# Performance work log

Hardware: AMD Instinct MI355X
Metric: run time of the kernel (lower is better)

The kernel has to match this reference:

```python
import jax, jax.numpy as jnp
import numpy as np


def _conv_bn_relu(x, w, b, stride):
    # Conv2d(k=3, pad=1) with eval-mode BatchNorm folded into (w, b) at setup, then ReLU.
    y = jax.lax.conv_general_dilated(x, w, (stride, stride), ((1, 1), (1, 1)),
                                     dimension_numbers=('NCHW', 'OIHW', 'NCHW'))
    return jax.nn.relu(y + b[None, :, None, None])


def _affine_grid(theta, H, W):
    # torch.nn.functional.affine_grid, align_corners=False
    xs = (2.0 * jnp.arange(W, dtype=theta.dtype) + 1.0) / W - 1.0  # [W]
    ys = (2.0 * jnp.arange(H, dtype=theta.dtype) + 1.0) / H - 1.0  # [H]
    gx = theta[:, 0, 0, None, None] * xs[None, None, :] + theta[:, 0, 1, None, None] * ys[None, :, None] + theta[:, 0, 2, None, None]
    gy = theta[:, 1, 0, None, None] * xs[None, None, :] + theta[:, 1, 1, None, None] * ys[None, :, None] + theta[:, 1, 2, None, None]
    return jnp.stack([gx, gy], axis=-1)  # [B,H,W,2]


def _grid_sample_bilinear_zeros(im, grid):
    # torch.nn.functional.grid_sample, mode='bilinear', padding_mode='zeros', align_corners=False
    B, C, H, W = im.shape
    ix = ((grid[..., 0] + 1.0) * W - 1.0) * 0.5  # [B,H,W] pixel x coords
    iy = ((grid[..., 1] + 1.0) * H - 1.0) * 0.5
    x0 = jnp.floor(ix); y0 = jnp.floor(iy)
    x1 = x0 + 1.0;      y1 = y0 + 1.0
    wx1 = ix - x0; wx0 = 1.0 - wx1
    wy1 = iy - y0; wy0 = 1.0 - wy1
    imt = jnp.transpose(im, (0, 2, 3, 1))  # BHWC for channel-last gather
    bidx = jnp.arange(B)[:, None, None]

    def gather(xf, yf):
        valid = ((xf >= 0) & (xf <= W - 1) & (yf >= 0) & (yf <= H - 1)).astype(im.dtype)
        xi = jnp.clip(xf.astype(jnp.int32), 0, W - 1)
        yi = jnp.clip(yf.astype(jnp.int32), 0, H - 1)
        return imt[bidx, yi, xi] * valid[..., None]  # [B,H,W,C]

    out = (gather(x0, y0) * (wx0 * wy0)[..., None]
           + gather(x1, y0) * (wx1 * wy0)[..., None]
           + gather(x0, y1) * (wx0 * wy1)[..., None]
           + gather(x1, y1) * (wx1 * wy1)[..., None])
    return jnp.transpose(out, (0, 3, 1, 2))  # back to NCHW


def _forward(im_tensor, w1, b1, w2, b2, w3, b3, w4, b4, w5, b5, w6, b6,
             fw1, fb1, fw2, fb2, fw3, fb3):
    B, _, H, W = im_tensor.shape
    x1 = _conv_bn_relu(im_tensor, w1, b1, 1)
    x2 = _conv_bn_relu(jnp.concatenate([x1, im_tensor], 1), w2, b2, 2)
    x3 = _conv_bn_relu(x2, w3, b3, 1)
    x4 = _conv_bn_relu(jnp.concatenate([x3, x2], 1), w4, b4, 2)
    x5 = _conv_bn_relu(x4, w5, b5, 1)
    xs = _conv_bn_relu(jnp.concatenate([x5, x4], 1), w6, b6, 2)
    xs = xs.reshape(B, -1)  # [B, 24*(H/8)*(W/8)]
    h = jax.nn.relu(xs @ fw1.T + fb1)
    h = jax.nn.relu(h @ fw2.T + fb2)
    sz = h @ fw3.T + fb3  # [B, 4]
    # mode == 'normal': vectorized theta construction (original loops over batch)
    theta = jnp.zeros((B, 2, 3), dtype=im_tensor.dtype)
    theta = theta.at[:, 0, 0].set(jax.nn.sigmoid(sz[:, 0]))
    theta = theta.at[:, 0, 2].set(jnp.tanh(sz[:, 2]))
    theta = theta.at[:, 1, 1].set(jax.nn.sigmoid(sz[:, 1]))
    theta = theta.at[:, 1, 2].set(jnp.tanh(sz[:, 3]))
    grid = _affine_grid(theta, H, W)
    im_cropped = _grid_sample_bilinear_zeros(im_tensor, grid)
    return im_cropped, theta


def setup_inputs() -> dict:
    key = jax.random.key(0)
    B, H, W = 32, 256, 256
    keys = iter(jax.random.split(key, 64))
    nk = lambda: next(keys)
    im = jax.random.normal(nk(), (B, 1, H, W), jnp.float32)

    def conv_params(cin, cout):
        w = jax.random.normal(nk(), (cout, cin, 3, 3), jnp.float32) * (1.0 / np.sqrt(cin * 9))
        b = jax.random.normal(nk(), (cout,), jnp.float32) * 0.01
        # eval-mode BatchNorm params, folded into conv weight/bias (exact same math)
        gamma = 1.0 + 0.1 * jax.random.normal(nk(), (cout,), jnp.float32)
        beta = 0.1 * jax.random.normal(nk(), (cout,), jnp.float32)
        mean = 0.1 * jax.random.normal(nk(), (cout,), jnp.float32)
        var = jnp.abs(1.0 + 0.1 * jax.random.normal(nk(), (cout,), jnp.float32))
        scale = gamma / jnp.sqrt(var + 1e-5)
        return w * scale[:, None, None, None], b * scale + (beta - mean * scale)

    w1, b1 = conv_params(1, 8)
    w2, b2 = conv_params(9, 8)
    w3, b3 = conv_params(8, 16)
    w4, b4 = conv_params(24, 16)
    w5, b5 = conv_params(16, 24)
    w6, b6 = conv_params(40, 24)
    feat = 24 * (H // 8) * (W // 8)
    fw1 = jax.random.normal(nk(), (1024, feat), jnp.float32) * (1.0 / np.sqrt(feat))
    fb1 = jnp.zeros((1024,), jnp.float32)
    fw2 = jax.random.normal(nk(), (32, 1024), jnp.float32) * (1.0 / np.sqrt(1024))
    fb2 = jnp.zeros((32,), jnp.float32)
    fw3 = jax.random.normal(nk(), (4, 32), jnp.float32) * 0.01  # small perturbation of zero-init
    fb3 = jnp.array([1.0, 1.0, 0.0, 0.0], jnp.float32)
    return dict(im_tensor=im, w1=w1, b1=b1, w2=w2, b2=b2, w3=w3, b3=b3,
                w4=w4, b4=b4, w5=w5, b5=b5, w6=w6, b6=b6,
                fw1=fw1, fb1=fb1, fw2=fw2, fb2=fb2, fw3=fw3, fb3=fb3)


def reference(im_tensor, w1, b1, w2, b2, w3, b3, w4, b4, w5, b5, w6, b6,
              fw1, fb1, fw2, fb2, fw3, fb3):
    return _forward(im_tensor, w1, b1, w2, b2, w3, b3, w4, b4, w5, b5, w6, b6,
                    fw1, fb1, fw2, fb2, fw3, fb3)
```

## Files before the change

### kernel.cpp

```cpp
#include <hip/hip_runtime.h>
#include <hip/hip_bf16.h>

template <int CIN1, int CIN2, int COUT, int CG, int CCH, int MINW>
__global__ __launch_bounds__(256, MINW) void convq_k(
    const float* __restrict__ in1, const float* __restrict__ in2,
    const float* __restrict__ w,
    const float* __restrict__ bias,
    float* __restrict__ out,
    int Hin, int Win)
{
    constexpr int CIN = CIN1 + CIN2;
    constexpr int NG  = COUT / CG;
    constexpr int NCH = CIN / CCH;
    constexpr int P   = 34;
    constexpr int NF4 = 10;
    constexpr int WL  = NF4 * 4;
    constexpr int E4  = CCH * P * NF4;
    constexpr int NLD = (E4 + 255) / 256;
    __shared__ __align__(16) float Xs[2][CCH][P][WL];

    const int Ho = Hin, Wo = Win;
    const int tpr = Wo / 32, tpc = Ho / 32;
    int bid = blockIdx.x;
    const int tx = bid % tpr; bid /= tpr;
    const int ty = bid % tpc; bid /= tpc;
    const int g  = bid % NG;  bid /= NG;
    const int b  = bid;
    const int cbase = g * CG;

    const int tid = threadIdx.x;
    const int lx = tid & 15, ly = tid >> 4;

    const int y0 = ty * 32 - 1;
    const int xA = tx * 32 - 4;
    const int HW = Hin * Win;

    float acc[CG][4];
#pragma unroll
    for (int co = 0; co < CG; ++co) {
        float bv = bias[cbase + co];
#pragma unroll
        for (int p = 0; p < 4; ++p) acc[co][p] = bv;
    }

    int cA[NLD], lOff[NLD], em[NLD];
    bool eok[NLD], rowk[NLD], f4[NLD];
    const float* b1p[NLD];
    const float* b2p[NLD];
#pragma unroll
    for (int l = 0; l < NLD; ++l) {
        int e = tid + l * 256;
        eok[l] = (e < E4);
        int ee = eok[l] ? e : 0;
        int c  = ee / (P * NF4), r = ee % (P * NF4);
        int py = r / NF4,        jx = r % NF4;
        cA[l]   = c;
        lOff[l] = ee;
        int gy = y0 + py, c0 = xA + jx * 4;
        rowk[l] = eok[l] && ((unsigned)gy < (unsigned)Hin);
        f4[l]   = (c0 >= 0) && (c0 + 4 <= Win);
        em[l] = 0;
#pragma unroll
        for (int e2 = 0; e2 < 4; ++e2)
            if ((unsigned)(c0 + e2) < (unsigned)Win) em[l] |= 1 << e2;
        b1p[l] = (const float*)((const char*)in1 +
                 ((ptrdiff_t)(b * CIN1 + c) * HW + (ptrdiff_t)gy * Win + c0)
                 * (ptrdiff_t)sizeof(float));
        b2p[l] = (CIN2 > 0)
            ? (const float*)((const char*)in2 +
                 ((ptrdiff_t)(b * CIN2 + c - CIN1) * HW + (ptrdiff_t)gy * Win + c0)
                 * (ptrdiff_t)sizeof(float))
            : b1p[l];
    }

    float4 stg[NLD];

    auto issue = [&](int cc) {
        const size_t adv = (size_t)cc * HW;
#pragma unroll
        for (int l = 0; l < NLD; ++l) {
            float4 v = {0.0f, 0.0f, 0.0f, 0.0f};
            if (rowk[l]) {
                int ci = cc + cA[l];
                const float* p = (CIN2 == 0 || ci < CIN1) ? (b1p[l] + adv)
                                                          : (b2p[l] + adv);
                if (f4[l]) {
                    v = *(const float4*)p;
                } else {
                    float* vp = reinterpret_cast<float*>(&v);
#pragma unroll
                    for (int e2 = 0; e2 < 4; ++e2)
                        if (em[l] & (1 << e2)) vp[e2] = p[e2];
                }
            }
            stg[l] = v;
        }
    };
    auto commit = [&](int bf) {
        float4* dst = (float4*)&Xs[0][0][0][0] + (size_t)bf * (CCH * P * NF4);
#pragma unroll
        for (int l = 0; l < NLD; ++l)
            if (eok[l]) dst[lOff[l]] = stg[l];
    };

    issue(0);
    commit(0);
    __syncthreads();

    const int cb = 2 * lx + 3;

    int buf = 0;
    for (int ch = 0; ch < NCH; ++ch) {
        if (ch + 1 < NCH) issue((ch + 1) * CCH);
#pragma unroll
        for (int c = 0; c < CCH; ++c) {
#pragma unroll
            for (int ky = 0; ky < 3; ++ky) {
                const float* x0 = &Xs[buf][c][2 * ly + ky][cb];
                const float* x1 = &Xs[buf][c][2 * ly + ky + 1][cb];
                float a0 = x0[0], a1 = x0[1], a2 = x0[2], a3 = x0[3];
                float b0 = x1[0], b1v = x1[1], b2v = x1[2], b3 = x1[3];
#pragma unroll
                for (int co = 0; co < CG; ++co) {
                    const float* wp = w +
                        ((size_t)(cbase + co) * CIN + ch * CCH + c) * 9 + ky * 3;
                    float w0 = wp[0], w1 = wp[1], w2 = wp[2];
                    acc[co][0] = fmaf(a0, w0, acc[co][0]);
                    acc[co][0] = fmaf(a1, w1, acc[co][0]);
                    acc[co][0] = fmaf(a2, w2, acc[co][0]);
                    acc[co][1] = fmaf(a1, w0, acc[co][1]);
                    acc[co][1] = fmaf(a2, w1, acc[co][1]);
                    acc[co][1] = fmaf(a3, w2, acc[co][1]);
                    acc[co][2] = fmaf(b0, w0, acc[co][2]);
                    acc[co][2] = fmaf(b1v, w1, acc[co][2]);
                    acc[co][2] = fmaf(b2v, w2, acc[co][2]);
                    acc[co][3] = fmaf(b1v, w0, acc[co][3]);
                    acc[co][3] = fmaf(b2v, w1, acc[co][3]);
                    acc[co][3] = fmaf(b3, w2, acc[co][3]);
                }
            }
        }
        if (ch + 1 < NCH) {
            commit(buf ^ 1);
            __syncthreads();
            buf ^= 1;
        }
    }

    const int oy = ty * 32 + 2 * ly;
    const int ox = tx * 32 + 2 * lx;
#pragma unroll
    for (int co = 0; co < CG; ++co)
#pragma unroll
        for (int dy = 0; dy < 2; ++dy) {
            float2 v;
            v.x = fmaxf(acc[co][dy * 2 + 0], 0.0f);
            v.y = fmaxf(acc[co][dy * 2 + 1], 0.0f);
            *(float2*)&out[((size_t)(b * COUT + cbase + co) * Ho + oy + dy) * Wo + ox] = v;
        }
}

template <int CIN1, int CIN2, int COUT, int CG, int STRIDE, int CCH, int MINW>
__global__ __launch_bounds__(256, MINW) void conv2p_k(
    const float* __restrict__ in1, const float* __restrict__ in2,
    const float* __restrict__ w,
    const float* __restrict__ bias,
    float* __restrict__ out,
    int Hin, int Win)
{
    constexpr int CIN = CIN1 + CIN2;
    constexpr int NG  = COUT / CG;
    constexpr int NCH = CIN / CCH;
    constexpr int P   = 16 * STRIDE + 2;
    constexpr int NF4 = (STRIDE == 1) ? 10 : 17;
    constexpr int WL  = NF4 * 4;
    constexpr int E4  = CCH * P * NF4;
    constexpr int NLD = (E4 + 255) / 256;
    __shared__ __align__(16) float Xs[2][CCH][P][WL];

    const int Ho = Hin / STRIDE, Wo = Win / STRIDE;
    const int tpr = Wo / 32, tpc = Ho / 16;
    int bid = blockIdx.x;
    const int tx = bid % tpr; bid /= tpr;
    const int ty = bid % tpc; bid /= tpc;
    const int g  = bid % NG;  bid /= NG;
    const int b  = bid;
    const int cbase = g * CG;

    const int tid = threadIdx.x;
    const int lx = tid & 15, ly = tid >> 4;

    const int y0 = ty * 16 * STRIDE - 1;
    const int xA = tx * 32 * STRIDE - 4;
    const int HW = Hin * Win;

    float2 acc[CG];
#pragma unroll
    for (int co = 0; co < CG; ++co) {
        float bv = bias[cbase + co];
        acc[co].x = bv; acc[co].y = bv;
    }

    int cA[NLD], lOff[NLD], em[NLD];
    bool eok[NLD], rowk[NLD], f4[NLD];
    const float* b1p[NLD];
    const float* b2p[NLD];
#pragma unroll
    for (int l = 0; l < NLD; ++l) {
        int e = tid + l * 256;
        eok[l] = (e < E4);
        int ee = eok[l] ? e : 0;
        int c  = ee / (P * NF4), r = ee % (P * NF4);
        int py = r / NF4,        jx = r % NF4;
        cA[l]   = c;
        lOff[l] = ee;
        int gy = y0 + py, c0 = xA + jx * 4;
        rowk[l] = eok[l] && ((unsigned)gy < (unsigned)Hin);
        f4[l]   = (c0 >= 0) && (c0 + 4 <= Win);
        em[l] = 0;
#pragma unroll
        for (int e2 = 0; e2 < 4; ++e2)
            if ((unsigned)(c0 + e2) < (unsigned)Win) em[l] |= 1 << e2;
        b1p[l] = (const float*)((const char*)in1 +
                 ((ptrdiff_t)(b * CIN1 + c) * HW + (ptrdiff_t)gy * Win + c0)
                 * (ptrdiff_t)sizeof(float));
        b2p[l] = (CIN2 > 0)
            ? (const float*)((const char*)in2 +
                 ((ptrdiff_t)(b * CIN2 + c - CIN1) * HW + (ptrdiff_t)gy * Win + c0)
                 * (ptrdiff_t)sizeof(float))
            : b1p[l];
    }

    float4 stg[NLD];

    auto issue = [&](int cc) {
        const size_t adv = (size_t)cc * HW;
#pragma unroll
        for (int l = 0; l < NLD; ++l) {
            float4 v = {0.0f, 0.0f, 0.0f, 0.0f};
            if (rowk[l]) {
                int ci = cc + cA[l];
                const float* p = (CIN2 == 0 || ci < CIN1) ? (b1p[l] + adv)
                                                          : (b2p[l] + adv);
                if (f4[l]) {
                    v = *(const float4*)p;
                } else {
                    float* vp = reinterpret_cast<float*>(&v);
#pragma unroll
                    for (int e2 = 0; e2 < 4; ++e2)
                        if (em[l] & (1 << e2)) vp[e2] = p[e2];
                }
            }
            stg[l] = v;
        }
    };
    auto commit = [&](int bf) {
        float4* dst = (float4*)&Xs[0][0][0][0] + (size_t)bf * (CCH * P * NF4);
#pragma unroll
        for (int l = 0; l < NLD; ++l)
            if (eok[l]) dst[lOff[l]] = stg[l];
    };

    issue(0);
    commit(0);
    __syncthreads();

    const int cb = (2 * lx) * STRIDE + 3;

    int buf = 0;
    for (int ch = 0; ch < NCH; ++ch) {
        if (ch + 1 < NCH) issue((ch + 1) * CCH);
#pragma unroll
        for (int c = 0; c < CCH; ++c) {
#pragma unroll
            for (int ky = 0; ky < 3; ++ky) {
                const float* xr = &Xs[buf][c][ly * STRIDE + ky][0];
                float2 r0, r1, r2;
                r0.x = xr[cb + 0]; r0.y = xr[cb + 0 + STRIDE];
                r1.x = xr[cb + 1]; r1.y = xr[cb + 1 + STRIDE];
                r2.x = xr[cb + 2]; r2.y = xr[cb + 2 + STRIDE];
#pragma unroll
                for (int co = 0; co < CG; ++co) {
                    const float* wp = w +
                        ((size_t)(cbase + co) * CIN + ch * CCH + c) * 9 + ky * 3;
                    float w0 = wp[0], w1 = wp[1], w2 = wp[2];
                    float2 a = acc[co];
                    a.x = fmaf(r0.x, w0, a.x); a.y = fmaf(r0.y, w0, a.y);
                    a.x = fmaf(r1.x, w1, a.x); a.y = fmaf(r1.y, w1, a.y);
                    a.x = fmaf(r2.x, w2, a.x); a.y = fmaf(r2.y, w2, a.y);
                    acc[co] = a;
                }
            }
        }
        if (ch + 1 < NCH) {
            commit(buf ^ 1);
            __syncthreads();
            buf ^= 1;
        }
    }

    const int oy = ty * 16 + ly;
    const int ox = tx * 32 + 2 * lx;
#pragma unroll
    for (int co = 0; co < CG; ++co) {
        float2 v;
        v.x = fmaxf(acc[co].x, 0.0f);
        v.y = fmaxf(acc[co].y, 0.0f);
        *(float2*)&out[((size_t)(b * COUT + cbase + co) * Ho + oy) * Wo + ox] = v;
    }
}

#define FC1_K 24576
#define FC1_N 1024
#define FC1_M 32
#define FC1_KS 32
#define FC1_KC 768
#define FC1_KP 64
#define FC1_NT 64

__global__ __launch_bounds__(256) void fc1_stage_k(
    const float* __restrict__ xs,
    const float* __restrict__ fw1,
    float* __restrict__ part)
{
    __shared__ __align__(16) float As[FC1_KP][36];
    __shared__ __align__(16) float Bs[FC1_KP][66];

    const int tid = threadIdx.x;
    const int n0 = blockIdx.x * FC1_NT;
    const int ks = blockIdx.y;
    const int k0 = ks * FC1_KC;
    const int lane = tid & 63;
    const int grp = tid >> 6;

    const int m4 = (tid & 7) * 4;
    const int n2 = (tid >> 3) * 2;

    float acc[4][2];
#pragma unroll
    for (int i = 0; i < 4; ++i)
#pragma unroll
        for (int j = 0; j < 2; ++j) acc[i][j] = 0.0f;

    for (int p = 0; p < FC1_KC / FC1_KP; ++p) {
        const int kc = k0 + p * FC1_KP;
#pragma unroll
        for (int r = 0; r < 8; ++r) {
            int m = grp * 8 + r;
            As[lane][m] = xs[(size_t)m * FC1_K + kc + lane];
        }
#pragma unroll
        for (int r = 0; r < 16; ++r) {
            int nl = grp * 16 + r;
            Bs[lane][nl] = fw1[(size_t)(n0 + nl) * FC1_K + kc + lane];
        }
        __syncthreads();
#pragma unroll 8
        for (int k = 0; k < FC1_KP; ++k) {
            float4 a = *(const float4*)&As[k][m4];
            float2 bv = *(const float2*)&Bs[k][n2];
            acc[0][0] += a.x * bv.x; acc[0][1] += a.x * bv.y;
            acc[1][0] += a.y * bv.x; acc[1][1] += a.y * bv.y;
            acc[2][0] += a.z * bv.x; acc[2][1] += a.z * bv.y;
            acc[3][0] += a.w * bv.x; acc[3][1] += a.w * bv.y;
        }
        __syncthreads();
    }
#pragma unroll
    for (int i = 0; i < 4; ++i)
#pragma unroll
        for (int j = 0; j < 2; ++j)
            part[((size_t)ks * FC1_M + (m4 + i)) * FC1_N + n0 + n2 + j] = acc[i][j];
}

__global__ __launch_bounds__(256) void fc1_reduce_k(
    const float* __restrict__ part, const float* __restrict__ fb1,
    float* __restrict__ h1)
{
    int idx = blockIdx.x * 256 + threadIdx.x;
    int n = idx & (FC1_N - 1);
    int m = idx >> 10;
    float s = fb1[n];
#pragma unroll
    for (int ks = 0; ks < FC1_KS; ++ks)
        s += part[((size_t)ks * FC1_M + m) * FC1_N + n];
    h1[idx] = fmaxf(s, 0.0f);
}

__global__ __launch_bounds__(256) void fc2_k(
    const float* __restrict__ h1, const float* __restrict__ fw2,
    const float* __restrict__ fb2, float* __restrict__ h2)
{
    __shared__ float hs[1024];
    const int m = blockIdx.x;
    const int tid = threadIdx.x;
    for (int i = tid; i < 1024; i += 256) hs[i] = h1[m * 1024 + i];
    __syncthreads();
    const int wave = tid >> 6, lane = tid & 63;
#pragma unroll 1
    for (int nn = 0; nn < 8; ++nn) {
        int n = wave * 8 + nn;
        float p = 0.0f;
        for (int k = lane; k < 1024; k += 64)
            p += fw2[n * 1024 + k] * hs[k];
#pragma unroll
        for (int off = 32; off; off >>= 1) p += __shfl_xor(p, off);
        if (lane == 0) h2[m * 32 + n] = fmaxf(p + fb2[n], 0.0f);
    }
}

__global__ void fc3_theta_k(
    const float* __restrict__ h2, const float* __restrict__ fw3,
    const float* __restrict__ fb3, float* __restrict__ theta_out)
{
    int t = threadIdx.x;
    if (t >= 128) return;
    int m = t >> 2, j = t & 3;
    float s = fb3[j];
#pragma unroll
    for (int k = 0; k < 32; ++k) s += h2[m * 32 + k] * fw3[j * 32 + k];
    float* th = theta_out + m * 6;
    if (j == 0)      { th[0] = 1.0f / (1.0f + expf(-s)); th[1] = 0.0f; }
    else if (j == 1) { th[4] = 1.0f / (1.0f + expf(-s)); th[3] = 0.0f; }
    else if (j == 2) { th[2] = tanhf(s); }
    else             { th[5] = tanhf(s); }
}

__global__ __launch_bounds__(256) void sampler_k(
    const float* __restrict__ im, const float* __restrict__ theta,
    float* __restrict__ out)
{
    int idx = blockIdx.x * 256 + threadIdx.x;
    int x = idx & 255;
    int y = (idx >> 8) & 255;
    int b = idx >> 16;
    const float* th = theta + b * 6;
    float xsn = (2.0f * x + 1.0f) * (1.0f / 256.0f) - 1.0f;
    float ysn = (2.0f * y + 1.0f) * (1.0f / 256.0f) - 1.0f;
    float gx = th[0] * xsn + th[1] * ysn + th[2];
    float gy = th[3] * xsn + th[4] * ysn + th[5];
    float ix = ((gx + 1.0f) * 256.0f - 1.0f) * 0.5f;
    float iy = ((gy + 1.0f) * 256.0f - 1.0f) * 0.5f;
    float x0 = floorf(ix), y0 = floorf(iy);
    float wx1 = ix - x0, wy1 = iy - y0;
    float wx0 = 1.0f - wx1, wy0 = 1.0f - wy1;
    const float* src = im + (size_t)b * 65536;

    auto g = [&](float xf, float yf) -> float {
        if (xf < 0.0f || xf > 255.0f || yf < 0.0f || yf > 255.0f) return 0.0f;
        int xi = (int)xf, yi = (int)yf;
        return src[yi * 256 + xi];
    };
    float v00 = g(x0, y0);
    float v10 = g(x0 + 1.0f, y0);
    float v01 = g(x0, y0 + 1.0f);
    float v11 = g(x0 + 1.0f, y0 + 1.0f);
    out[idx] = v00 * wx0 * wy0 + v10 * wx1 * wy0 + v01 * wx0 * wy1 + v11 * wx1 * wy1;
}

extern "C" void kernel_launch(void* const* d_in, const int* in_sizes, int n_in,
                              void* d_out, int out_size, void* d_ws, size_t ws_size,
                              hipStream_t stream)
{
    const float* im  = (const float*)d_in[0];
    const float* w1  = (const float*)d_in[1];  const float* b1 = (const float*)d_in[2];
    const float* w2  = (const float*)d_in[3];  const float* b2 = (const float*)d_in[4];
    const float* w3  = (const float*)d_in[5];  const float* b3 = (const float*)d_in[6];
    const float* w4  = (const float*)d_in[7];  const float* b4 = (const float*)d_in[8];
    const float* w5  = (const float*)d_in[9];  const float* b5 = (const float*)d_in[10];
    const float* w6  = (const float*)d_in[11]; const float* b6 = (const float*)d_in[12];
    const float* fw1 = (const float*)d_in[13]; const float* fb1 = (const float*)d_in[14];
    const float* fw2 = (const float*)d_in[15]; const float* fb2 = (const float*)d_in[16];
    const float* fw3 = (const float*)d_in[17]; const float* fb3 = (const float*)d_in[18];

    float* out = (float*)d_out;
    float* ws  = (float*)d_ws;

    float* x2   = ws + 0;
    float* x1c  = ws + 4194304;
    float* x3   = ws + 4194304;
    float* x4   = ws + 12582912;
    float* x5   = ws + 4194304;
    float* x6   = ws + 14680064;
    float* part = ws + 0;
    float* h1   = ws + 1048576;
    float* h2   = ws + 1081344;

    float* theta = out + 32 * 65536;

    for (int c = 0; c < 2; ++c) {
        const float* imc = im + (size_t)c * 16 * 65536;
        convq_k<1, 0, 8, 8, 1, 4><<<16 * 1 * 8 * 8, 256, 0, stream>>>(
            imc, nullptr, w1, b1, x1c, 256, 256);
        conv2p_k<8, 1, 8, 8, 2, 1, 6><<<16 * 8 * 4, 256, 0, stream>>>(
            x1c, imc, w2, b2, x2 + (size_t)c * 2097152, 256, 256);
    }
    convq_k<8, 0, 16, 8, 2, 4><<<32 * 2 * 4 * 4, 256, 0, stream>>>(
        x2, nullptr, w3, b3, x3, 128, 128);
    conv2p_k<16, 8, 16, 4, 2, 1, 6><<<32 * 4 * 2 * 4, 256, 0, stream>>>(
        x3, x2, w4, b4, x4, 128, 128);
    convq_k<16, 0, 24, 6, 2, 4><<<32 * 4 * 2 * 2, 256, 0, stream>>>(
        x4, nullptr, w5, b5, x5, 64, 64);
    conv2p_k<24, 16, 24, 4, 2, 1, 6><<<32 * 2 * 1 * 6, 256, 0, stream>>>(
        x5, x4, w6, b6, x6, 64, 64);

    fc1_stage_k<<<dim3(16, FC1_KS), 256, 0, stream>>>(x6, fw1, part);
    fc1_reduce_k<<<128, 256, 0, stream>>>(part, fb1, h1);
    fc2_k<<<32, 256, 0, stream>>>(h1, fw2, fb2, h2);
    fc3_theta_k<<<1, 128, 0, stream>>>(h2, fw3, fb3, theta);

    sampler_k<<<8192, 256, 0, stream>>>(im, theta, out);
}
```

Baseline: 281.8 us.

## Add 2x2-per-thread stride-2 conv kernel for conv4 and conv6

Adds a stride-2 conv kernel in which each thread computes a 2x2 block of outputs from a 66-row by 72-column shared tile, one input channel per stage, using double buffering and register-staged prefetch. Conv4 and conv6 switch from the generic conv2p kernel to this one. Each thread reuses the loaded input row values across two horizontally adjacent outputs, so fewer shared-memory reads are issued per FMA. In exchange there are fewer blocks (conv6 launches only 256), the per-block tile is larger, and occupancy and parallelism may drop.

```diff
diff --git a/kernel.cpp b/kernel.cpp
--- a/kernel.cpp
+++ b/kernel.cpp
@@ -160,6 +160,157 @@
         }
 }
 
+template <int CIN1, int CIN2, int COUT, int CG, int MINW>
+__global__ __launch_bounds__(256, MINW) void convq2_k(
+    const float* __restrict__ in1, const float* __restrict__ in2,
+    const float* __restrict__ w,
+    const float* __restrict__ bias,
+    float* __restrict__ out,
+    int Hin, int Win)
+{
+    constexpr int CIN = CIN1 + CIN2;
+    constexpr int NG  = COUT / CG;
+    constexpr int P   = 66;
+    constexpr int NF4 = 18;
+    constexpr int WL  = NF4 * 4;
+    constexpr int E4  = P * NF4;
+    constexpr int NLD = (E4 + 255) / 256;
+    __shared__ __align__(16) float Xs[2][P][WL];
+
+    const int Ho = Hin / 2, Wo = Win / 2;
+    const int tpr = Wo / 32, tpc = Ho / 32;
+    int bid = blockIdx.x;
+    const int tx = bid % tpr; bid /= tpr;
+    const int ty = bid % tpc; bid /= tpc;
+    const int g  = bid % NG;  bid /= NG;
+    const int b  = bid;
+    const int cbase = g * CG;
+
+    const int tid = threadIdx.x;
+    const int lx = tid & 15, ly = tid >> 4;
+
+    const int y0 = ty * 64 - 1;
+    const int xA = tx * 64 - 4;
+    const int HW = Hin * Win;
+
+    float acc[CG][4];
+#pragma unroll
+    for (int co = 0; co < CG; ++co) {
+        float bv = bias[cbase + co];
+#pragma unroll
+        for (int p = 0; p < 4; ++p) acc[co][p] = bv;
+    }
+
+    int lOff[NLD], em[NLD];
+    bool eok[NLD], rowk[NLD], f4[NLD];
+    const float* b1p[NLD];
+    const float* b2p[NLD];
+#pragma unroll
+    for (int l = 0; l < NLD; ++l) {
+        int e = tid + l * 256;
+        eok[l] = (e < E4);
+        int ee = eok[l] ? e : 0;
+        int py = ee / NF4, jx = ee % NF4;
+        lOff[l] = ee;
+        int gy = y0 + py, c0 = xA + jx * 4;
+        rowk[l] = eok[l] && ((unsigned)gy < (unsigned)Hin);
+        f4[l]   = (c0 >= 0) && (c0 + 4 <= Win);
+        em[l] = 0;
+#pragma unroll
+        for (int e2 = 0; e2 < 4; ++e2)
+            if ((unsigned)(c0 + e2) < (unsigned)Win) em[l] |= 1 << e2;
+        b1p[l] = (const float*)((const char*)in1 +
+                 ((ptrdiff_t)(b * CIN1) * HW + (ptrdiff_t)gy * Win + c0)
+                 * (ptrdiff_t)sizeof(float));
+        b2p[l] = (CIN2 > 0)
+            ? (const float*)((const char*)in2 +
+                 ((ptrdiff_t)(b * CIN2 - CIN1) * HW + (ptrdiff_t)gy * Win + c0)
+                 * (ptrdiff_t)sizeof(float))
+            : b1p[l];
+    }
+
+    float4 stg[NLD];
+
+    auto issue = [&](int ci) {
+        const size_t adv = (size_t)ci * HW;
+#pragma unroll
+        for (int l = 0; l < NLD; ++l) {
+            float4 v = {0.0f, 0.0f, 0.0f, 0.0f};
+            if (rowk[l]) {
+                const float* p = (CIN2 == 0 || ci < CIN1) ? (b1p[l] + adv)
+                                                          : (b2p[l] + adv);
+                if (f4[l]) {
+                    v = *(const float4*)p;
+                } else {
+                    float* vp = reinterpret_cast<float*>(&v);
+#pragma unroll
+                    for (int e2 = 0; e2 < 4; ++e2)
+                        if (em[l] & (1 << e2)) vp[e2] = p[e2];
+                }
+            }
+            stg[l] = v;
+        }
+    };
+    auto commit = [&](int bf) {
+        float4* dst = (float4*)&Xs[0][0][0] + (size_t)bf * E4;
+#pragma unroll
+        for (int l = 0; l < NLD; ++l)
+            if (eok[l]) dst[lOff[l]] = stg[l];
+    };
+
+    issue(0);
+    commit(0);
+    __syncthreads();
+
+    const int cb = 4 * lx + 3;
+
+    int buf = 0;
+    for (int ch = 0; ch < CIN; ++ch) {
+        if (ch + 1 < CIN) issue(ch + 1);
+#pragma unroll
+        for (int ky = 0; ky < 3; ++ky) {
+            const float* x0 = &Xs[buf][4 * ly + ky][cb];
+            const float* x1 = &Xs[buf][4 * ly + ky + 2][cb];
+            float v0 = x0[0], v1 = x0[1], v2 = x0[2], v3 = x0[3], v4 = x0[4];
+            float u0 = x1[0], u1 = x1[1], u2 = x1[2], u3 = x1[3], u4 = x1[4];
+#pragma unroll
+            for (int co = 0; co < CG; ++co) {
+                const float* wp = w + ((size_t)(cbase + co) * CIN + ch) * 9 + ky * 3;
+                float w0 = wp[0], w1 = wp[1], w2 = wp[2];
+                acc[co][0] = fmaf(v0, w0, acc[co][0]);
+                acc[co][0] = fmaf(v1, w1, acc[co][0]);
+                acc[co][0] = fmaf(v2, w2, acc[co][0]);
+                acc[co][1] = fmaf(v2, w0, acc[co][1]);
+                acc[co][1] = fmaf(v3, w1, acc[co][1]);
+                acc[co][1] = fmaf(v4, w2, acc[co][1]);
+                acc[co][2] = fmaf(u0, w0, acc[co][2]);
+                acc[co][2] = fmaf(u1, w1, acc[co][2]);
+                acc[co][2] = fmaf(u2, w2, acc[co][2]);
+                acc[co][3] = fmaf(u2, w0, acc[co][3]);
+                acc[co][3] = fmaf(u3, w1, acc[co][3]);
+                acc[co][3] = fmaf(u4, w2, acc[co][3]);
+            }
+        }
+        if (ch + 1 < CIN) {
+            commit(buf ^ 1);
+            __syncthreads();
+            buf ^= 1;
+        }
+    }
+
+    const int oy = ty * 32 + 2 * ly;
+    const int ox = tx * 32 + 2 * lx;
+#pragma unroll
+    for (int co = 0; co < CG; ++co)
+#pragma unroll
+        for (int dy = 0; dy < 2; ++dy) {
+            float2 v;
+            v.x = fmaxf(acc[co][dy * 2 + 0], 0.0f);
+            v.y = fmaxf(acc[co][dy * 2 + 1], 0.0f);
+            *(float2*)&out[((size_t)(b * COUT + cbase + co) * Ho + oy + dy) * Wo + ox] = v;
+        }
+}
+
 template <int CIN1, int CIN2, int COUT, int CG, int STRIDE, int CCH, int MINW>
 __global__ __launch_bounds__(256, MINW) void conv2p_k(
     const float* __restrict__ in1, const float* __restrict__ in2,
@@ -497,11 +648,11 @@
     }
     convq_k<8, 0, 16, 8, 2, 4><<<32 * 2 * 4 * 4, 256, 0, stream>>>(
         x2, nullptr, w3, b3, x3, 128, 128);
-    conv2p_k<16, 8, 16, 4, 2, 1, 6><<<32 * 4 * 2 * 4, 256, 0, stream>>>(
+    convq2_k<16, 8, 16, 4, 4><<<32 * 4 * 2 * 2, 256, 0, stream>>>(
         x3, x2, w4, b4, x4, 128, 128);
     convq_k<16, 0, 24, 6, 2, 4><<<32 * 4 * 2 * 2, 256, 0, stream>>>(
         x4, nullptr, w5, b5, x5, 64, 64);
-    conv2p_k<24, 16, 24, 4, 2, 1, 6><<<32 * 2 * 1 * 6, 256, 0, stream>>>(
+    convq2_k<24, 16, 24, 3, 4><<<32 * 8 * 1 * 1, 256, 0, stream>>>(
         x5, x4, w6, b6, x6, 64, 64);
 
     fc1_stage_k<<<dim3(16, FC1_KS), 256, 0, stream>>>(x6, fw1, part);
```

Measured after the change: 307.6 us. 9.2% more time.
